# Optimization experiments

Hardware: AMD Instinct MI355X
Metric: run time of the kernel (lower is better)

The kernel has to match this reference:

```python
import jax, jax.numpy as jnp
import numpy as np

D_IN, D_HEAD, D_EXPAND, D_OUT, H = 512, 64, 2048, 512, 8
D_Q = D_HEAD * H  # 512
D_K = D_HEAD * H  # 512
D_V = D_IN * H    # 4096 (non-standard: per-head value dim = d_in)
EPS = 1e-5


def layernorm(x, g, b):
    mu = jnp.mean(x, axis=-1, keepdims=True)
    var = jnp.mean(jnp.square(x - mu), axis=-1, keepdims=True)
    return (x - mu) * jax.lax.rsqrt(var + EPS) * g + b


def setup_inputs() -> dict:
    key = jax.random.key(0)
    ks = jax.random.split(key, 12)
    B, N = 2, 2048
    s_in = 1.0 / np.sqrt(D_IN)
    s_mh = 1.0 / np.sqrt(D_IN * H)
    s_ex = 1.0 / np.sqrt(D_EXPAND)
    return {
        "x": jax.random.normal(ks[0], (B, N, D_IN), jnp.float32),
        "ln1_g": jnp.ones((D_IN,), jnp.float32),
        "ln1_b": jnp.zeros((D_IN,), jnp.float32),
        "Wqkv": jax.random.normal(ks[1], (D_IN, D_Q + D_K + D_V), jnp.float32) * s_in,
        "bqkv": jax.random.normal(ks[2], (D_Q + D_K + D_V,), jnp.float32) * 0.01,
        "Wm": jax.random.normal(ks[3], (D_IN * H, D_IN), jnp.float32) * s_mh,
        "bm": jax.random.normal(ks[4], (D_IN,), jnp.float32) * 0.01,
        "ln2_g": jnp.ones((D_IN,), jnp.float32),
        "ln2_b": jnp.zeros((D_IN,), jnp.float32),
        "W1": jax.random.normal(ks[5], (D_IN, D_EXPAND), jnp.float32) * s_in,
        "b1": jax.random.normal(ks[6], (D_EXPAND,), jnp.float32) * 0.01,
        "W2": jax.random.normal(ks[7], (D_EXPAND, D_OUT), jnp.float32) * s_ex,
        "b2": jax.random.normal(ks[8], (D_OUT,), jnp.float32) * 0.01,
    }


def reference(x, ln1_g, ln1_b, Wqkv, bqkv, Wm, bm, ln2_g, ln2_b, W1, b1, W2, b2):
    B, N, _ = x.shape
    scale = D_HEAD ** -0.5
    qkv = layernorm(x, ln1_g, ln1_b) @ Wqkv + bqkv
    q, k, v = jnp.split(qkv, [D_Q, D_Q + D_K], axis=-1)
    q = q.reshape(B, N, H, D_HEAD).transpose(0, 2, 1, 3)  # (B,H,N,dh)
    k = k.reshape(B, N, H, D_HEAD).transpose(0, 2, 1, 3)
    v = v.reshape(B, N, H, D_IN).transpose(0, 2, 1, 3)    # (B,H,N,d_in)
    attn = jax.nn.softmax(jnp.einsum('bhnd,bhmd->bhnm', q, k) * scale, axis=-1)
    out = jnp.einsum('bhnm,bhmc->bhnc', attn, v)          # (B,H,N,d_in)
    out = out.transpose(0, 2, 1, 3).reshape(B, N, H * D_IN)
    x2 = x + out @ Wm + bm
    h = layernorm(x2, ln2_g, ln2_b) @ W1 + b1
    h = h * jax.nn.sigmoid(h)  # Swish
    return h @ W2 + b2 + x2    # shortcut = Identity (d_in == d_out)
```

## Files before the change

### kernel.cpp

```cpp
#include <hip/hip_runtime.h>
#include <cmath>

typedef unsigned short u16;
typedef unsigned int   u32;
typedef __attribute__((ext_vector_type(8))) __bf16 bf16x8;
typedef __attribute__((ext_vector_type(4))) float  f32x4;
typedef __attribute__((ext_vector_type(8))) unsigned short u16x8;
typedef __attribute__((ext_vector_type(4))) unsigned short u16x4;

#define DEV __device__ __forceinline__

DEV float bf2f(u16 u){ union{u32 i; float f;} v; v.i=((u32)u)<<16; return v.f; }
DEV u16 f2bf(float f){ union{float f; u32 i;} v; v.f=f; u32 r=v.i+0x7fffu+((v.i>>16)&1u); return (u16)(r>>16); }

#if defined(__has_builtin) && __has_builtin(__builtin_amdgcn_global_load_lds)
DEV void gld16(const void* g, void* l){
  __builtin_amdgcn_global_load_lds((__attribute__((address_space(1))) void*)g,
                                   (__attribute__((address_space(3))) void*)l, 16, 0, 0);
}
#else
DEV void gld16(const void* g, void* l){ *(u16x8*)l = *(const u16x8*)g; }
#endif

#if defined(__has_builtin) && __has_builtin(__builtin_amdgcn_exp2f)
DEV float fexp2(float x){ return __builtin_amdgcn_exp2f(x); }
#else
DEV float fexp2(float x){ return exp2f(x); }
#endif

__global__ void detect_k(const u16* __restrict__ x, int* __restrict__ flag)
{
  if (threadIdx.x == 0 && blockIdx.x == 0){
    int sane = 0;
    for (int i = 0; i < 64; ++i){
      int e = (x[i] >> 7) & 0xFF;
      sane += (e >= 100 && e <= 150);
    }
    *flag = (sane < 56) ? 1 : 0;
  }
}

__global__ __launch_bounds__(256)
void conv_vecs(const void* a0,const void* a1,const void* a2,const void* a3,
               const void* a4,const void* a5,const void* a6,const void* a7,
               float* __restrict__ dst, const int* __restrict__ flag)
{
  int i = blockIdx.x*256 + threadIdx.x;
  if (i >= 10240) return;
  const void* src; int off;
  if      (i < 512)  { src=a0; off=i; }
  else if (i < 1024) { src=a1; off=i-512; }
  else if (i < 6144) { src=a2; off=i-1024; }
  else if (i < 6656) { src=a3; off=i-6144; }
  else if (i < 7168) { src=a4; off=i-6656; }
  else if (i < 7680) { src=a5; off=i-7168; }
  else if (i < 9728) { src=a6; off=i-7680; }
  else               { src=a7; off=i-9728; }
  dst[i] = (*flag) ? ((const float*)src)[off] : bf2f(((const u16*)src)[off]);
}

#define SWZ_SRC(c) (((c)&7) ^ (((c)>>3)&7))

template<int MODE>
__global__ __launch_bounds__(256)
void gemm_bt(const u16* __restrict__ A, const u16* __restrict__ BT,
             void* __restrict__ C, const float* __restrict__ bias,
             int K, int lda, int ldb, int ldc)
{
  __shared__ u16 As[128*64];
  __shared__ u16 Bs[128*64];
  const int tid  = threadIdx.x;
  const int lane = tid & 63;
  const int quad = lane>>4, l7 = lane&7, l15 = lane&15;
  const int wv   = tid >> 6;
  const int wm   = wv >> 1, wn = wv & 1;
  const long m0 = (long)blockIdx.y * 128;
  const long n0 = (long)blockIdx.x * 128;

  f32x4 acc[4][4];
#pragma unroll
  for (int i=0;i<4;i++)
#pragma unroll
    for (int j=0;j<4;j++) acc[i][j] = (f32x4){0.f,0.f,0.f,0.f};

  for (int k0=0; k0<K; k0+=64){
    __syncthreads();
#pragma unroll
    for (int i=0;i<4;i++){
      int c = i*256 + tid;
      gld16(A  + (m0 + (c>>3))*lda + k0 + SWZ_SRC(c)*8, &As[c*8]);
      gld16(BT + (n0 + (c>>3))*ldb + k0 + SWZ_SRC(c)*8, &Bs[c*8]);
    }
    __syncthreads();
#pragma unroll
    for (int kk=0;kk<2;kk++){
      const int ch = ((kk*4 + quad) ^ l7) * 8;
      bf16x8 af[4], bfr[4];
#pragma unroll
      for (int t=0;t<4;t++){
        af[t]  = *(const bf16x8*)&As[(wm*64 + t*16 + l15)*64 + ch];
        bfr[t] = *(const bf16x8*)&Bs[(wn*64 + t*16 + l15)*64 + ch];
      }
#pragma unroll
      for (int ti=0;ti<4;ti++)
#pragma unroll
        for (int tj=0;tj<4;tj++)
          acc[ti][tj] = __builtin_amdgcn_mfma_f32_16x16x32_bf16(af[ti], bfr[tj], acc[ti][tj], 0,0,0);
    }
  }

#pragma unroll
  for (int ti=0;ti<4;ti++)
#pragma unroll
  for (int tj=0;tj<4;tj++)
#pragma unroll
  for (int r=0;r<4;r++){
    long row = m0 + wm*64 + ti*16 + quad*4 + r;
    long col = n0 + wn*64 + tj*16 + l15;
    float v = acc[ti][tj][r] + bias[col];
    if (MODE==2) v = v / (1.f + __expf(-v));
    ((u16*)C)[row*ldc+col] = f2bf(v);
  }
}

template<int MODE>
__global__ __launch_bounds__(256)
void gemm_n64(const u16* __restrict__ A, const u16* __restrict__ BT,
              void* __restrict__ C, const float* __restrict__ bias,
              const void* __restrict__ res,
              int K, int lda, int ldb, int ldc, const int* __restrict__ flag)
{
  __shared__ u16 As[128*64];
  __shared__ u16 Bs[64*64];
  const int tid  = threadIdx.x;
  const int lane = tid & 63;
  const int quad = lane>>4, l7 = lane&7, l15 = lane&15;
  const int wm   = tid >> 6;
  const long m0 = (long)blockIdx.y * 128;
  const long n0 = (long)blockIdx.x * 64;
  const bool f32io = flag && (*flag != 0);

  f32x4 acc[2][4];
#pragma unroll
  for (int i=0;i<2;i++)
#pragma unroll
    for (int j=0;j<4;j++) acc[i][j] = (f32x4){0.f,0.f,0.f,0.f};

  for (int k0=0; k0<K; k0+=64){
    __syncthreads();
#pragma unroll
    for (int i=0;i<4;i++){
      int c = i*256 + tid;
      gld16(A + (m0 + (c>>3))*lda + k0 + SWZ_SRC(c)*8, &As[c*8]);
    }
#pragma unroll
    for (int i=0;i<2;i++){
      int c = i*256 + tid;
      gld16(BT + (n0 + (c>>3))*ldb + k0 + SWZ_SRC(c)*8, &Bs[c*8]);
    }
    __syncthreads();
#pragma unroll
    for (int kk=0;kk<2;kk++){
      const int ch = ((kk*4 + quad) ^ l7) * 8;
      bf16x8 af[2], bfr[4];
#pragma unroll
      for (int t=0;t<2;t++)
        af[t]  = *(const bf16x8*)&As[(wm*32 + t*16 + l15)*64 + ch];
#pragma unroll
      for (int t=0;t<4;t++)
        bfr[t] = *(const bf16x8*)&Bs[(t*16 + l15)*64 + ch];
#pragma unroll
      for (int ti=0;ti<2;ti++)
#pragma unroll
        for (int tj=0;tj<4;tj++)
          acc[ti][tj] = __builtin_amdgcn_mfma_f32_16x16x32_bf16(af[ti], bfr[tj], acc[ti][tj], 0,0,0);
    }
  }

#pragma unroll
  for (int ti=0;ti<2;ti++)
#pragma unroll
  for (int tj=0;tj<4;tj++)
#pragma unroll
  for (int r=0;r<4;r++){
    long row = m0 + wm*32 + ti*16 + quad*4 + r;
    long col = n0 + tj*16 + l15;
    float v = acc[ti][tj][r] + bias[col];
    if (MODE==1){
      v += f32io ? ((const float*)res)[row*ldc+col]
                 : bf2f(((const u16*)res)[row*ldc+col]);
      ((float*)C)[row*ldc+col] = v;
    } else {
      v += ((const float*)res)[row*ldc+col];
      if (f32io) ((float*)C)[row*ldc+col] = v;
      else       ((u16*)C)[row*ldc+col]   = f2bf(v);
    }
  }
}

__global__ __launch_bounds__(512, 2)
void att_flash(const u16* __restrict__ qkv, const u16* __restrict__ vt,
               u16* __restrict__ ao)
{
  __shared__ u16 Qs[128*64];
  __shared__ u16 Ks[2][64*64];
  __shared__ u16 Ps[128*68];
  __shared__ u16 Vs[512*64];
  __shared__ float m_run[128], l_run[128], alph[128];
  __shared__ int resc[2];
  const int tid=threadIdx.x, lane=tid&63, wv=tid>>6;
  const int wm=wv>>2, wn=wv&3;
  const int quad=lane>>4, l7=lane&7, l15=lane&15;
  const int bid = blockIdx.x;
  const int id  = ((bid&7)<<5) + (bid>>3);
  const int qt  = id & 15, bh = id >> 4;
  const int b = bh>>3, h = bh&7;
  const long q0 = (long)qt*128;
  const u16* qb = qkv + ((long)b*2048 + q0)*5120 + h*64;
  const u16* kb = qkv + (long)b*2048*5120 + 512 + h*64;
  const u16* vb = vt + (long)bh*512*2048;

#pragma unroll
  for (int i=0;i<2;i++){
    int c=i*512+tid;
    gld16(qb + (long)(c>>3)*5120 + SWZ_SRC(c)*8, &Qs[c*8]);
  }
  { int c=tid; gld16(kb + (long)(c>>3)*5120 + SWZ_SRC(c)*8, &Ks[0][c*8]); }
  if (tid<128){ m_run[tid] = -1e30f; l_run[tid] = 0.f; }
  if (tid==0){ resc[0]=0; resc[1]=0; }

  f32x4 o[4][8];
#pragma unroll
  for (int i=0;i<4;i++)
#pragma unroll
    for (int j=0;j<8;j++) o[i][j] = (f32x4){0.f,0.f,0.f,0.f};

  for (int mt=0; mt<32; ++mt){
    const long m0 = (long)mt*64;
    const int cur = mt&1;
    __syncthreads();

    if (mt < 31){ int c=tid; gld16(kb + (m0+64 + (c>>3))*5120 + SWZ_SRC(c)*8, &Ks[cur^1][c*8]); }
#pragma unroll
    for (int i=0;i<8;i++){
      int c=i*512+tid;
      gld16(vb + (long)(c>>3)*2048 + m0 + SWZ_SRC(c)*8, &Vs[c*8]);
    }
    if (tid==0) resc[cur^1] = 0;

    f32x4 s[4];
#pragma unroll
    for (int j=0;j<4;j++) s[j] = (f32x4){0.f,0.f,0.f,0.f};
#pragma unroll
    for (int kk=0;kk<2;kk++){
      const int ch = ((kk*4 + quad) ^ l7) * 8;
      bf16x8 af = *(const bf16x8*)&Qs[(wv*16 + l15)*64 + ch];
#pragma unroll
      for (int tj=0;tj<4;tj++){
        bf16x8 bfr = *(const bf16x8*)&Ks[cur][(tj*16 + l15)*64 + ch];
        s[tj] = __builtin_amdgcn_mfma_f32_16x16x32_bf16(af, bfr, s[tj], 0,0,0);
      }
    }

    float nm[4], al[4], rs[4];
    bool chg = false;
#pragma unroll
    for (int r=0;r<4;r++){
      float vm = fmaxf(fmaxf(s[0][r],s[1][r]), fmaxf(s[2][r],s[3][r]));
      vm = fmaxf(vm, __shfl_xor(vm,1)); vm = fmaxf(vm, __shfl_xor(vm,2));
      vm = fmaxf(vm, __shfl_xor(vm,4)); vm = fmaxf(vm, __shfl_xor(vm,8));
      float mo = m_run[wv*16 + quad*4 + r];
      float vs = vm*0.125f;
      bool c_ = (vs > mo + 8.f);
      nm[r] = c_ ? vs : mo;
      al[r] = c_ ? __expf(mo - vs) : 1.f;
      chg |= c_;
      rs[r] = 0.f;
    }
    float nml[4];
#pragma unroll
    for (int r=0;r<4;r++) nml[r] = nm[r]*1.44269504f;
#pragma unroll
    for (int tj=0;tj<4;tj++)
#pragma unroll
    for (int r=0;r<4;r++){
      float pv = fexp2(fmaf(s[tj][r], 0.18033688f, -nml[r]));
      rs[r] += pv;
      Ps[(wv*16 + quad*4 + r)*68 + tj*16 + l15] = f2bf(pv);
    }
#pragma unroll
    for (int r=0;r<4;r++){
      rs[r] += __shfl_xor(rs[r],1); rs[r] += __shfl_xor(rs[r],2);
      rs[r] += __shfl_xor(rs[r],4); rs[r] += __shfl_xor(rs[r],8);
    }
    if (l15==0){
#pragma unroll
      for (int r=0;r<4;r++){
        int row = wv*16 + quad*4 + r;
        alph[row]  = al[r];
        m_run[row] = nm[r];
        l_run[row] = l_run[row]*al[r] + rs[r];
      }
    }
    if (__any((int)chg) && lane==0) resc[cur] = 1;
    __syncthreads();

    if (resc[cur]){
      float a_[4][4];
#pragma unroll
      for (int ti=0;ti<4;ti++)
#pragma unroll
        for (int r=0;r<4;r++) a_[ti][r] = alph[wm*64 + ti*16 + quad*4 + r];
#pragma unroll
      for (int ti=0;ti<4;ti++)
#pragma unroll
      for (int tj=0;tj<8;tj++)
#pragma unroll
        for (int r=0;r<4;r++) o[ti][tj][r] *= a_[ti][r];
    }
#pragma unroll
    for (int kk=0;kk<2;kk++){
      const int ch = ((kk*4 + quad) ^ l7) * 8;
      bf16x8 af[4], bfr[8];
#pragma unroll
      for (int t=0;t<4;t++){
        int base = (wm*64 + t*16 + l15)*68 + kk*32 + quad*8;
        union { u16x4 hh[2]; bf16x8 v; } u;
        u.hh[0] = *(const u16x4*)&Ps[base];
        u.hh[1] = *(const u16x4*)&Ps[base+4];
        af[t] = u.v;
      }
#pragma unroll
      for (int t=0;t<8;t++)
        bfr[t] = *(const bf16x8*)&Vs[(wn*128 + t*16 + l15)*64 + ch];
#pragma unroll
      for (int ti=0;ti<4;ti++)
#pragma unroll
        for (int tj=0;tj<8;tj++)
          o[ti][tj] = __builtin_amdgcn_mfma_f32_16x16x32_bf16(af[ti], bfr[tj], o[ti][tj], 0,0,0);
    }
  }

  float rl[4][4];
#pragma unroll
  for (int ti=0;ti<4;ti++)
#pragma unroll
    for (int r=0;r<4;r++) rl[ti][r] = 1.f / l_run[wm*64 + ti*16 + quad*4 + r];
#pragma unroll
  for (int ti=0;ti<4;ti++)
#pragma unroll
  for (int tj=0;tj<8;tj++)
#pragma unroll
  for (int r=0;r<4;r++){
    long rown = q0 + wm*64 + ti*16 + quad*4 + r;
    long col  = wn*128 + tj*16 + l15;
    ao[((long)b*2048 + rown)*4096 + (long)h*512 + col] = f2bf(o[ti][tj][r]*rl[ti][r]);
  }
}

template<int SRC>
__global__ __launch_bounds__(256)
void ln_kernel(const void* __restrict__ xin, const float* __restrict__ g,
               const float* __restrict__ bb, u16* __restrict__ out,
               const int* __restrict__ flag)
{
  const int tid=threadIdx.x, lane=tid&63, wv=tid>>6;
  const long row = (long)blockIdx.x*4 + wv;
  const bool f32 = (SRC==1) || (flag && *flag != 0);
  float v[8];
  if (f32){
    const float* xr = (const float*)xin + row*512 + lane*8;
#pragma unroll
    for (int j=0;j<8;j++) v[j]=xr[j];
  } else {
    const u16* xr = (const u16*)xin + row*512 + lane*8;
    u16x8 xv = *(const u16x8*)xr;
#pragma unroll
    for (int j=0;j<8;j++) v[j]=bf2f(xv[j]);
  }
  float s1=0.f, s2=0.f;
#pragma unroll
  for (int j=0;j<8;j++){ s1+=v[j]; s2+=v[j]*v[j]; }
  for (int off=1; off<64; off<<=1){ s1+=__shfl_xor(s1,off); s2+=__shfl_xor(s2,off); }
  float mu  = s1*(1.f/512.f);
  float var = s2*(1.f/512.f) - mu*mu;
  float rs  = rsqrtf(var + 1e-5f);
  u16x8 ov;
#pragma unroll
  for (int j=0;j<8;j++){
    int col = lane*8+j;
    ov[j] = f2bf((v[j]-mu)*rs*g[col] + bb[col]);
  }
  *(u16x8*)(out + row*512 + lane*8) = ov;
}

template<bool DUAL>
__global__ __launch_bounds__(256)
void transpose_k(const void* __restrict__ in_, u16* __restrict__ out,
                 int ldi, int ldo, long izh, long izl, long oz,
                 const int* __restrict__ flag)
{
  __shared__ u16 t[32][33];
  const int z = blockIdx.z;
  const bool f32 = DUAL && flag && (*flag != 0);
  const long zoff = (long)(z>>3)*izh + (long)(z&7)*izl;
  out += (long)z*oz;
  const int tx = threadIdx.x, ty = threadIdx.y;
  const long c  = (long)blockIdx.x*32 + tx;
  const long r0 = (long)blockIdx.y*32;
  if (f32){
    const float* in = (const float*)in_ + zoff;
#pragma unroll
    for (int j=0;j<4;j++) t[ty+j*8][tx] = f2bf(in[(r0+ty+j*8)*ldi + c]);
  } else {
    const u16* in = (const u16*)in_ + zoff;
#pragma unroll
    for (int j=0;j<4;j++) t[ty+j*8][tx] = in[(r0+ty+j*8)*ldi + c];
  }
  __syncthreads();
  const long rr = r0 + tx;
  const long cc = (long)blockIdx.x*32 + ty;
#pragma unroll
  for (int j=0;j<4;j++) out[(cc+j*8)*ldo + rr] = t[tx][ty+j*8];
}

extern "C" void kernel_launch(void* const* d_in, const int* in_sizes, int n_in,
                              void* d_out, int out_size, void* d_ws, size_t ws_size,
                              hipStream_t stream)
{
  const void* x    = d_in[0];
  const void* ln1g = d_in[1];
  const void* ln1b = d_in[2];
  const void* Wqkv = d_in[3];
  const void* bqkv = d_in[4];
  const void* Wm   = d_in[5];
  const void* bm   = d_in[6];
  const void* ln2g = d_in[7];
  const void* ln2b = d_in[8];
  const void* W1   = d_in[9];
  const void* b1   = d_in[10];
  const void* W2   = d_in[11];
  const void* b2   = d_in[12];

  char* p = (char*)d_ws;
  auto take = [&](size_t n){ void* r=(void*)p; p += (n + 255) & ~(size_t)255; return r; };
  u16*   lnb   = (u16*)  take((size_t)4096*512*2);
  u16*   qkv   = (u16*)  take((size_t)4096*5120*2);
  u16*   vtb   = (u16*)  take((size_t)16*512*2048*2);
  u16*   wqkvT = (u16*)  take((size_t)5120*512*2);
  u16*   wmT   = (u16*)  take((size_t)512*4096*2);
  u16*   w1T   = (u16*)  take((size_t)2048*512*2);
  u16*   w2T   = (u16*)  take((size_t)512*2048*2);
  u16*   ao    = (u16*)  take((size_t)4096*4096*2);
  float* cvec  = (float*)take((size_t)10240*4);
  int*   flag  = (int*)  take(4);
  float* x2    = (float*)vtb;
  u16*   hb    = qkv;

  detect_k<<<1, 64, 0, stream>>>((const u16*)x, flag);
  conv_vecs<<<40, 256, 0, stream>>>(ln1g, ln1b, bqkv, bm, ln2g, ln2b, b1, b2, cvec, flag);

  dim3 tb(32,8);
  transpose_k<true><<<dim3(160,16,1), tb, 0, stream>>>(Wqkv, wqkvT, 5120, 512, 0,0,0, flag);
  transpose_k<true><<<dim3(16,128,1), tb, 0, stream>>>(Wm,   wmT,   512, 4096, 0,0,0, flag);
  transpose_k<true><<<dim3(64,16,1),  tb, 0, stream>>>(W1,   w1T,  2048, 512, 0,0,0, flag);
  transpose_k<true><<<dim3(16,64,1),  tb, 0, stream>>>(W2,   w2T,   512, 2048, 0,0,0, flag);

  ln_kernel<0><<<1024, 256, 0, stream>>>(x, cvec+0, cvec+512, lnb, flag);
  gemm_bt<0><<<dim3(40,32), 256, 0, stream>>>(lnb, wqkvT, qkv, cvec+1024, 512, 512, 512, 5120);

  transpose_k<false><<<dim3(16,64,16), tb, 0, stream>>>(qkv + 1024, vtb, 5120, 2048,
                                                        (long)2048*5120, 512, (long)512*2048, nullptr);
  att_flash<<<dim3(256), 512, 0, stream>>>(qkv, vtb, ao);

  gemm_n64<1><<<dim3(8,32), 256, 0, stream>>>(ao, wmT, x2, cvec+6144, x,
                                              4096, 4096, 4096, 512, flag);
  ln_kernel<1><<<1024, 256, 0, stream>>>(x2, cvec+6656, cvec+7168, lnb, nullptr);
  gemm_bt<2><<<dim3(16,32), 256, 0, stream>>>(lnb, w1T, hb, cvec+7680, 512, 512, 512, 2048);
  gemm_n64<3><<<dim3(8,32), 256, 0, stream>>>(hb, w2T, d_out, cvec+9728, x2,
                                              2048, 2048, 2048, 512, flag);
}
```

Measured before the change: 415.8 us.

## Double-buffer V tiles, keep Q in registers, prefetch K via registers in attention

The attention kernel now keeps Q fragments in registers instead of shared memory, which frees LDS for a double-buffered V tile. The next V tile is prefetched asynchronously while the current tile is used. The next K tile is loaded into registers and written to a single K buffer after the mid-iteration barrier. The P conversion to bf16 switches to a cheaper round-half-up formula instead of round-to-nearest-even. This aims to overlap V/K global loads with compute, at the cost of more register pressure and LDS use (Vs grows to 128KB), which may reduce occupancy below the 2 blocks per CU requested by the launch bounds.

New measurement: 409.1 us. About the same (-1.6%).

```diff
diff --git a/kernel.cpp b/kernel.cpp
--- a/kernel.cpp
+++ b/kernel.cpp
@@ -12,6 +12,7 @@
 
 DEV float bf2f(u16 u){ union{u32 i; float f;} v; v.i=((u32)u)<<16; return v.f; }
 DEV u16 f2bf(float f){ union{float f; u32 i;} v; v.f=f; u32 r=v.i+0x7fffu+((v.i>>16)&1u); return (u16)(r>>16); }
+DEV u16 f2bf_fast(float f){ union{float f; u32 i;} v; v.f=f; return (u16)((v.i + 0x8000u)>>16); }
 
 #if defined(__has_builtin) && __has_builtin(__builtin_amdgcn_global_load_lds)
 DEV void gld16(const void* g, void* l){
@@ -202,10 +203,9 @@
 void att_flash(const u16* __restrict__ qkv, const u16* __restrict__ vt,
                u16* __restrict__ ao)
 {
-  __shared__ u16 Qs[128*64];
-  __shared__ u16 Ks[2][64*64];
+  __shared__ u16 Ks[64*64];
   __shared__ u16 Ps[128*68];
-  __shared__ u16 Vs[512*64];
+  __shared__ u16 Vs[2][512*64];
   __shared__ float m_run[128], l_run[128], alph[128];
   __shared__ int resc[2];
   const int tid=threadIdx.x, lane=tid&63, wv=tid>>6;
@@ -220,12 +220,17 @@
   const u16* kb = qkv + (long)b*2048*5120 + 512 + h*64;
   const u16* vb = vt + (long)bh*512*2048;
 
-#pragma unroll
-  for (int i=0;i<2;i++){
+  bf16x8 qreg[2];
+#pragma unroll
+  for (int kk=0;kk<2;kk++)
+    qreg[kk] = *(const bf16x8*)(qb + (long)(wv*16 + l15)*5120 + (kk*4+quad)*8);
+
+  { int c=tid; gld16(kb + (long)(c>>3)*5120 + SWZ_SRC(c)*8, &Ks[c*8]); }
+#pragma unroll
+  for (int i=0;i<8;i++){
     int c=i*512+tid;
-    gld16(qb + (long)(c>>3)*5120 + SWZ_SRC(c)*8, &Qs[c*8]);
-  }
-  { int c=tid; gld16(kb + (long)(c>>3)*5120 + SWZ_SRC(c)*8, &Ks[0][c*8]); }
+    gld16(vb + (long)(c>>3)*2048 + SWZ_SRC(c)*8, &Vs[0][c*8]);
+  }
   if (tid<128){ m_run[tid] = -1e30f; l_run[tid] = 0.f; }
   if (tid==0){ resc[0]=0; resc[1]=0; }
 
@@ -235,16 +240,21 @@
 #pragma unroll
     for (int j=0;j<8;j++) o[i][j] = (f32x4){0.f,0.f,0.f,0.f};
 
+  __syncthreads();
+
+  int buf = 0;
   for (int mt=0; mt<32; ++mt){
-    const long m0 = (long)mt*64;
     const int cur = mt&1;
-    __syncthreads();
-
-    if (mt < 31){ int c=tid; gld16(kb + (m0+64 + (c>>3))*5120 + SWZ_SRC(c)*8, &Ks[cur^1][c*8]); }
-#pragma unroll
-    for (int i=0;i<8;i++){
-      int c=i*512+tid;
-      gld16(vb + (long)(c>>3)*2048 + m0 + SWZ_SRC(c)*8, &Vs[c*8]);
+
+    u16x8 kreg = {};
+    if (mt < 31){
+      const long m1 = (long)(mt+1)*64;
+      { int c=tid; kreg = *(const u16x8*)(kb + (m1 + (c>>3))*5120 + SWZ_SRC(c)*8); }
+#pragma unroll
+      for (int i=0;i<8;i++){
+        int c=i*512+tid;
+        gld16(vb + (long)(c>>3)*2048 + m1 + SWZ_SRC(c)*8, &Vs[buf^1][c*8]);
+      }
     }
     if (tid==0) resc[cur^1] = 0;
 
@@ -254,11 +264,10 @@
 #pragma unroll
     for (int kk=0;kk<2;kk++){
       const int ch = ((kk*4 + quad) ^ l7) * 8;
-      bf16x8 af = *(const bf16x8*)&Qs[(wv*16 + l15)*64 + ch];
 #pragma unroll
       for (int tj=0;tj<4;tj++){
-        bf16x8 bfr = *(const bf16x8*)&Ks[cur][(tj*16 + l15)*64 + ch];
-        s[tj] = __builtin_amdgcn_mfma_f32_16x16x32_bf16(af, bfr, s[tj], 0,0,0);
+        bf16x8 bfr = *(const bf16x8*)&Ks[(tj*16 + l15)*64 + ch];
+        s[tj] = __builtin_amdgcn_mfma_f32_16x16x32_bf16(qreg[kk], bfr, s[tj], 0,0,0);
       }
     }
 
@@ -286,7 +295,7 @@
     for (int r=0;r<4;r++){
       float pv = fexp2(fmaf(s[tj][r], 0.18033688f, -nml[r]));
       rs[r] += pv;
-      Ps[(wv*16 + quad*4 + r)*68 + tj*16 + l15] = f2bf(pv);
+      Ps[(wv*16 + quad*4 + r)*68 + tj*16 + l15] = f2bf_fast(pv);
     }
 #pragma unroll
     for (int r=0;r<4;r++){
@@ -303,7 +312,11 @@
       }
     }
     if (__any((int)chg) && lane==0) resc[cur] = 1;
-    __syncthreads();
+
+    asm volatile("s_waitcnt lgkmcnt(0)" ::: "memory");
+    __builtin_amdgcn_s_barrier();
+
+    if (mt < 31){ int c=tid; *(u16x8*)&Ks[c*8] = kreg; }
 
     if (resc[cur]){
       float a_[4][4];
@@ -332,13 +345,16 @@
       }
 #pragma unroll
       for (int t=0;t<8;t++)
-        bfr[t] = *(const bf16x8*)&Vs[(wn*128 + t*16 + l15)*64 + ch];
+        bfr[t] = *(const bf16x8*)&Vs[buf][(wn*128 + t*16 + l15)*64 + ch];
 #pragma unroll
       for (int ti=0;ti<4;ti++)
 #pragma unroll
         for (int tj=0;tj<8;tj++)
           o[ti][tj] = __builtin_amdgcn_mfma_f32_16x16x32_bf16(af[ti], bfr[tj], o[ti][tj], 0,0,0);
     }
+
+    __syncthreads();
+    buf ^= 1;
   }
 
   float rl[4][4];
```

## Double-buffer gemm_n64 LDS tiles and remap blocks across XCDs for locality

Applied to the files above, without the earlier changes.

The N=64 GEMM kernel now uses two LDS buffers, so the global-to-LDS load of the next K tile is issued before computing on the current one, with a single barrier per iteration. That overlaps memory latency with MFMA work on the long-K GEMMs (K=4096 and K=2048). Separately, all GEMM launches remap block indices so that blocks scheduled round-robin onto the same XCD share A or B tiles, aiming for better L2 reuse. Double buffering doubles gemm_n64's LDS use (to 48KB), which may lower occupancy.

Measured after the change: 397.1 us. -4.5%, faster.

```diff
diff --git a/kernel.cpp b/kernel.cpp
--- a/kernel.cpp
+++ b/kernel.cpp
@@ -61,7 +61,25 @@
 
 #define SWZ_SRC(c) (((c)&7) ^ (((c)>>3)&7))
 
-template<int MODE>
+template<int SWZ>
+DEV void remap_xcd(int& bx, int& by)
+{
+  if (SWZ==1){
+    int L = by*(int)gridDim.x + bx;
+    int xcd = L & 7, l = L >> 3;
+    int chunk = (int)gridDim.x >> 3;
+    bx = xcd*chunk + (l % chunk);
+    by = l / chunk;
+  } else if (SWZ==2){
+    int L = by*(int)gridDim.x + bx;
+    int xcd = L & 7, l = L >> 3;
+    int chunk = (int)gridDim.y >> 3;
+    by = xcd*chunk + (l % chunk);
+    bx = l / chunk;
+  }
+}
+
+template<int MODE, int SWZ>
 __global__ __launch_bounds__(256)
 void gemm_bt(const u16* __restrict__ A, const u16* __restrict__ BT,
              void* __restrict__ C, const float* __restrict__ bias,
@@ -74,8 +92,10 @@
   const int quad = lane>>4, l7 = lane&7, l15 = lane&15;
   const int wv   = tid >> 6;
   const int wm   = wv >> 1, wn = wv & 1;
-  const long m0 = (long)blockIdx.y * 128;
-  const long n0 = (long)blockIdx.x * 128;
+  int bx = blockIdx.x, by = blockIdx.y;
+  remap_xcd<SWZ>(bx, by);
+  const long m0 = (long)by * 128;
+  const long n0 = (long)bx * 128;
 
   f32x4 acc[4][4];
 #pragma unroll
@@ -123,21 +143,23 @@
   }
 }
 
-template<int MODE>
+template<int MODE, int SWZ>
 __global__ __launch_bounds__(256)
 void gemm_n64(const u16* __restrict__ A, const u16* __restrict__ BT,
               void* __restrict__ C, const float* __restrict__ bias,
               const void* __restrict__ res,
               int K, int lda, int ldb, int ldc, const int* __restrict__ flag)
 {
-  __shared__ u16 As[128*64];
-  __shared__ u16 Bs[64*64];
+  __shared__ u16 As[2][128*64];
+  __shared__ u16 Bs[2][64*64];
   const int tid  = threadIdx.x;
   const int lane = tid & 63;
   const int quad = lane>>4, l7 = lane&7, l15 = lane&15;
   const int wm   = tid >> 6;
-  const long m0 = (long)blockIdx.y * 128;
-  const long n0 = (long)blockIdx.x * 64;
+  int bx = blockIdx.x, by = blockIdx.y;
+  remap_xcd<SWZ>(bx, by);
+  const long m0 = (long)by * 128;
+  const long n0 = (long)bx * 64;
   const bool f32io = flag && (*flag != 0);
 
   f32x4 acc[2][4];
@@ -146,35 +168,43 @@
 #pragma unroll
     for (int j=0;j<4;j++) acc[i][j] = (f32x4){0.f,0.f,0.f,0.f};
 
-  for (int k0=0; k0<K; k0+=64){
-    __syncthreads();
+  auto stage = [&](int bi, int k0){
 #pragma unroll
     for (int i=0;i<4;i++){
       int c = i*256 + tid;
-      gld16(A + (m0 + (c>>3))*lda + k0 + SWZ_SRC(c)*8, &As[c*8]);
+      gld16(A + (m0 + (c>>3))*lda + k0 + SWZ_SRC(c)*8, &As[bi][c*8]);
     }
 #pragma unroll
     for (int i=0;i<2;i++){
       int c = i*256 + tid;
-      gld16(BT + (n0 + (c>>3))*ldb + k0 + SWZ_SRC(c)*8, &Bs[c*8]);
-    }
-    __syncthreads();
+      gld16(BT + (n0 + (c>>3))*ldb + k0 + SWZ_SRC(c)*8, &Bs[bi][c*8]);
+    }
+  };
+
+  const int S = K >> 6;
+  stage(0, 0);
+  __syncthreads();
+
+  for (int s=0; s<S; ++s){
+    const int cb = s & 1;
+    if (s+1 < S) stage(cb^1, (s+1)<<6);
 #pragma unroll
     for (int kk=0;kk<2;kk++){
       const int ch = ((kk*4 + quad) ^ l7) * 8;
       bf16x8 af[2], bfr[4];
 #pragma unroll
       for (int t=0;t<2;t++)
-        af[t]  = *(const bf16x8*)&As[(wm*32 + t*16 + l15)*64 + ch];
+        af[t]  = *(const bf16x8*)&As[cb][(wm*32 + t*16 + l15)*64 + ch];
 #pragma unroll
       for (int t=0;t<4;t++)
-        bfr[t] = *(const bf16x8*)&Bs[(t*16 + l15)*64 + ch];
+        bfr[t] = *(const bf16x8*)&Bs[cb][(t*16 + l15)*64 + ch];
 #pragma unroll
       for (int ti=0;ti<2;ti++)
 #pragma unroll
         for (int tj=0;tj<4;tj++)
           acc[ti][tj] = __builtin_amdgcn_mfma_f32_16x16x32_bf16(af[ti], bfr[tj], acc[ti][tj], 0,0,0);
     }
+    __syncthreads();
   }
 
 #pragma unroll
@@ -467,16 +497,16 @@
   transpose_k<true><<<dim3(16,64,1),  tb, 0, stream>>>(W2,   w2T,   512, 2048, 0,0,0, flag);
 
   ln_kernel<0><<<1024, 256, 0, stream>>>(x, cvec+0, cvec+512, lnb, flag);
-  gemm_bt<0><<<dim3(40,32), 256, 0, stream>>>(lnb, wqkvT, qkv, cvec+1024, 512, 512, 512, 5120);
+  gemm_bt<0,1><<<dim3(40,32), 256, 0, stream>>>(lnb, wqkvT, qkv, cvec+1024, 512, 512, 512, 5120);
 
   transpose_k<false><<<dim3(16,64,16), tb, 0, stream>>>(qkv + 1024, vtb, 5120, 2048,
                                                         (long)2048*5120, 512, (long)512*2048, nullptr);
   att_flash<<<dim3(256), 512, 0, stream>>>(qkv, vtb, ao);
 
-  gemm_n64<1><<<dim3(8,32), 256, 0, stream>>>(ao, wmT, x2, cvec+6144, x,
-                                              4096, 4096, 4096, 512, flag);
+  gemm_n64<1,2><<<dim3(8,32), 256, 0, stream>>>(ao, wmT, x2, cvec+6144, x,
+                                                4096, 4096, 4096, 512, flag);
   ln_kernel<1><<<1024, 256, 0, stream>>>(x2, cvec+6656, cvec+7168, lnb, nullptr);
-  gemm_bt<2><<<dim3(16,32), 256, 0, stream>>>(lnb, w1T, hb, cvec+7680, 512, 512, 512, 2048);
-  gemm_n64<3><<<dim3(8,32), 256, 0, stream>>>(hb, w2T, d_out, cvec+9728, x2,
-                                              2048, 2048, 2048, 512, flag);
-}
+  gemm_bt<2,2><<<dim3(16,32), 256, 0, stream>>>(lnb, w1T, hb, cvec+7680, 512, 512, 512, 2048);
+  gemm_n64<3,2><<<dim3(8,32), 256, 0, stream>>>(hb, w2T, d_out, cvec+9728, x2,
+                                                2048, 2048, 2048, 512, flag);
+}
```
